# Kernel optimization log

Measured on AMD Instinct MI355X. Metric: run time of the kernel, lower is better.

Reference implementation:

```python
import jax, jax.numpy as jnp
import numpy as np

N_USER = 100000
N_ITEM = 100000
N_EDGE = 1600000
IN_U = 128
IN_I = 128
OUT = 64
NEG_SLOPE = 0.01  # torch F.leaky_relu default


def setup_inputs() -> dict:
    key = jax.random.key(0)
    ks = jax.random.split(key, 12)
    return {
        'feat_user': jax.random.normal(ks[0], (N_USER, IN_U), jnp.float32),
        'feat_item': jax.random.normal(ks[1], (N_ITEM, IN_I), jnp.float32),
        'W_user': jax.random.normal(ks[2], (IN_U, OUT), jnp.float32) * 0.05,
        'b_user': jax.random.normal(ks[3], (OUT,), jnp.float32) * 0.05,
        'W_item': jax.random.normal(ks[4], (IN_I, OUT), jnp.float32) * 0.05,
        'b_item': jax.random.normal(ks[5], (OUT,), jnp.float32) * 0.05,
        'attn_w': jax.random.normal(ks[6], (2 * OUT, 1), jnp.float32) * 0.05,
        'src_u2i': jax.random.randint(ks[7], (N_EDGE,), 0, N_USER),
        'dst_u2i': jax.random.randint(ks[8], (N_EDGE,), 0, N_ITEM),
        'src_i2u': jax.random.randint(ks[9], (N_EDGE,), 0, N_ITEM),
        'dst_i2u': jax.random.randint(ks[10], (N_EDGE,), 0, N_USER),
    }


def _segment_softmax(e, seg, num_segments):
    # e: [E], seg: [E] destination ids -> softmax over edges sharing a dst
    m = jax.ops.segment_max(e, seg, num_segments=num_segments)
    ex = jnp.exp(e - m[seg])
    s = jax.ops.segment_sum(ex, seg, num_segments=num_segments)
    return ex / s[seg]


def _etype_aggregate(Wh_src, Wh_dst, attn_w, src, dst, n_dst):
    # gather per-edge src/dst projected features: [E, OUT]
    zs = Wh_src[src]
    zd = Wh_dst[dst]
    # attn([zs || zd]) == zs @ a_src + zd @ a_dst (split the 2*OUT weight)
    a_src, a_dst = attn_w[:OUT, 0], attn_w[OUT:, 0]
    e = zs @ a_src + zd @ a_dst  # [E]
    e = jnp.where(e > 0, e, NEG_SLOPE * e)  # leaky_relu
    alpha = _segment_softmax(e, dst, n_dst)  # [E]
    # weighted scatter-sum into destination nodes
    return jax.ops.segment_sum(alpha[:, None] * zs, dst, num_segments=n_dst)


def reference(feat_user, feat_item, W_user, b_user, W_item, b_item, attn_w,
              src_u2i, dst_u2i, src_i2u, dst_i2u):
    Wh_user = feat_user @ W_user + b_user  # fc['user'] (etype 'user': user->item)
    Wh_item = feat_item @ W_item + b_item  # fc['item'] (etype 'item': item->user)
    # etype 'user': user -> item; dst attention feature is Wh_item on item nodes
    h_item = _etype_aggregate(Wh_user, Wh_item, attn_w, src_u2i, dst_u2i, N_ITEM)
    # etype 'item': item -> user
    h_user = _etype_aggregate(Wh_item, Wh_user, attn_w, src_i2u, dst_i2u, N_USER)
    # update_nodes sums all 'self_*' per ntype; each ntype has exactly one here
    return jnp.concatenate([h_user, h_item], axis=0)  # [N_USER+N_ITEM, OUT]
```

## Files before the change

### kernel.cpp

```cpp
#include <hip/hip_runtime.h>
#include <hip/hip_bf16.h>

#define NU 100000
#define NI 100000
#define NE 1600000
#define KIN 128
#define KOUT 64

#define NCOPY 8
#define PBK 128
#define NP 782
#define CAP2 384
#define CHUNK 4096
#define SRTSZ (NCOPY * CAP2 + PBK * 7)
#define AGG_THREADS 512
#define NWAVE 8

#define LIN_ROWS 64
#define LIN_GRID 512
#define LIN_ITERS 1563

__device__ __forceinline__ unsigned short f2bf(float f) {
    unsigned u = __float_as_uint(f);
    unsigned r = (u + 0x7fffu + ((u >> 16) & 1u)) >> 16;
    return (unsigned short)r;
}
__device__ __forceinline__ float bf2f(unsigned short h) {
    return __uint_as_float(((unsigned)h) << 16);
}

__global__ __launch_bounds__(256) void linear_attn_kernel(
    const float* __restrict__ A0, const float* __restrict__ W0, const float* __restrict__ bv0,
    const float* __restrict__ A1, const float* __restrict__ W1, const float* __restrict__ bv1,
    const float* __restrict__ attn,
    unsigned short* __restrict__ Wh0, float* __restrict__ su0, float* __restrict__ sd0,
    unsigned short* __restrict__ Wh1, float* __restrict__ su1, float* __restrict__ sd1)
{
    __shared__ float Wl[128 * 64];
    __shared__ float Al[LIN_ROWS * 132];

    int half = gridDim.x >> 1;
    bool second = blockIdx.x >= (unsigned)half;
    const float* A = second ? A1 : A0;
    const float* W = second ? W1 : W0;
    const float* bvec = second ? bv1 : bv0;
    unsigned short* Wh = second ? Wh1 : Wh0;
    float* s_src = second ? su1 : su0;
    float* s_dst = second ? sd1 : sd0;
    int blk = second ? (blockIdx.x - half) : blockIdx.x;

    int t = threadIdx.x;
    int c4 = t & 15;
    int rt = t >> 4;

    for (int i = t; i < 128 * 64 / 4; i += 256) ((float4*)Wl)[i] = ((const float4*)W)[i];

    float4 bias4 = *(const float4*)(bvec + c4 * 4);
    float4 as4   = *(const float4*)(attn + c4 * 4);
    float4 ad4   = *(const float4*)(attn + 64 + c4 * 4);

    for (int c = blk; c < LIN_ITERS; c += half) {
        int rowbase = c * LIN_ROWS;
        __syncthreads();
        for (int g = t; g < LIN_ROWS * 32; g += 256) {
            int rr = g >> 5;
            int q  = g & 31;
            float4 v = {0.f, 0.f, 0.f, 0.f};
            int grow = rowbase + rr;
            if (grow < NU) v = ((const float4*)(A + (size_t)grow * 128))[q];
            *(float4*)&Al[rr * 132 + q * 4] = v;
        }
        __syncthreads();

        float4 acc0 = bias4, acc1 = bias4, acc2 = bias4, acc3 = bias4;
        const float* Ar = &Al[rt * 132];
        const float* Wc = &Wl[c4 * 4];
        #pragma unroll 4
        for (int kq = 0; kq < 128; kq += 4) {
            float4 a0 = *(const float4*)&Ar[ 0 * 132 + kq];
            float4 a1 = *(const float4*)&Ar[16 * 132 + kq];
            float4 a2 = *(const float4*)&Ar[32 * 132 + kq];
            float4 a3 = *(const float4*)&Ar[48 * 132 + kq];
            float4 w0 = *(const float4*)&Wc[(kq + 0) * 64];
            float4 w1 = *(const float4*)&Wc[(kq + 1) * 64];
            float4 w2 = *(const float4*)&Wc[(kq + 2) * 64];
            float4 w3 = *(const float4*)&Wc[(kq + 3) * 64];
            acc0.x += a0.x*w0.x + a0.y*w1.x + a0.z*w2.x + a0.w*w3.x;
            acc0.y += a0.x*w0.y + a0.y*w1.y + a0.z*w2.y + a0.w*w3.y;
            acc0.z += a0.x*w0.z + a0.y*w1.z + a0.z*w2.z + a0.w*w3.z;
            acc0.w += a0.x*w0.w + a0.y*w1.w + a0.z*w2.w + a0.w*w3.w;
            acc1.x += a1.x*w0.x + a1.y*w1.x + a1.z*w2.x + a1.w*w3.x;
            acc1.y += a1.x*w0.y + a1.y*w1.y + a1.z*w2.y + a1.w*w3.y;
            acc1.z += a1.x*w0.z + a1.y*w1.z + a1.z*w2.z + a1.w*w3.z;
            acc1.w += a1.x*w0.w + a1.y*w1.w + a1.z*w2.w + a1.w*w3.w;
            acc2.x += a2.x*w0.x + a2.y*w1.x + a2.z*w2.x + a2.w*w3.x;
            acc2.y += a2.x*w0.y + a2.y*w1.y + a2.z*w2.y + a2.w*w3.y;
            acc2.z += a2.x*w0.z + a2.y*w1.z + a2.z*w2.z + a2.w*w3.z;
            acc2.w += a2.x*w0.w + a2.y*w1.w + a2.z*w2.w + a2.w*w3.w;
            acc3.x += a3.x*w0.x + a3.y*w1.x + a3.z*w2.x + a3.w*w3.x;
            acc3.y += a3.x*w0.y + a3.y*w1.y + a3.z*w2.y + a3.w*w3.y;
            acc3.z += a3.x*w0.z + a3.y*w1.z + a3.z*w2.z + a3.w*w3.z;
            acc3.w += a3.x*w0.w + a3.y*w1.w + a3.z*w2.w + a3.w*w3.w;
        }

        float4 accs[4] = {acc0, acc1, acc2, acc3};
        #pragma unroll
        for (int i = 0; i < 4; i++) {
            int row = rowbase + rt + 16 * i;
            float4 av = accs[i];
            if (row < NU) {
                ushort4 o;
                o.x = f2bf(av.x); o.y = f2bf(av.y); o.z = f2bf(av.z); o.w = f2bf(av.w);
                ((ushort4*)(Wh + (size_t)row * KOUT))[c4] = o;
            }
            float p1 = av.x*as4.x + av.y*as4.y + av.z*as4.z + av.w*as4.w;
            float p2 = av.x*ad4.x + av.y*ad4.y + av.z*ad4.z + av.w*ad4.w;
            #pragma unroll
            for (int off = 8; off; off >>= 1) {
                p1 += __shfl_down(p1, off, 16);
                p2 += __shfl_down(p2, off, 16);
            }
            if (c4 == 0 && row < NU) { s_src[row] = p1; s_dst[row] = p2; }
        }
    }
}

__global__ __launch_bounds__(256) void scatter_kernel(
    const int* __restrict__ src_u2i, const int* __restrict__ dst_u2i,
    const int* __restrict__ src_i2u, const int* __restrict__ dst_i2u,
    int* __restrict__ cur_item, int* __restrict__ cur_user,
    int* __restrict__ ebuf_item, int* __restrict__ ebuf_user,
    int nE, int nbs)
{
    __shared__ int raw[CHUNK];
    __shared__ unsigned short bkt[CHUNK];
    __shared__ int srt_[CHUNK];
    __shared__ unsigned short sbk[CHUNK];
    __shared__ int cnt[NP];
    __shared__ int gb[NP];
    __shared__ int pb[NP];
    __shared__ int lc[NP];

    bool u2i = blockIdx.x < (unsigned)nbs;
    int blk = u2i ? blockIdx.x : (blockIdx.x - nbs);
    int copy = blockIdx.x & (NCOPY - 1);
    const int* src = u2i ? src_u2i : src_i2u;
    const int* dst = u2i ? dst_u2i : dst_i2u;
    int* cur  = (u2i ? cur_item : cur_user) + copy * NP;
    int* ebuf = (u2i ? ebuf_item : ebuf_user) + (size_t)copy * NP * CAP2;

    int t = threadIdx.x;
    for (int i = t; i < NP; i += 256) cnt[i] = 0;
    __syncthreads();

    int e0 = blk * CHUNK;
    int n = nE - e0; if (n > CHUNK) n = CHUNK;

    for (int j = t; j < n; j += 256) {
        int s = src[e0 + j], d = dst[e0 + j];
        int b = d >> 7;
        raw[j] = s | ((d & 127) << 17);
        bkt[j] = (unsigned short)b;
        atomicAdd(&cnt[b], 1);
    }
    __syncthreads();

    for (int b = t; b < NP; b += 256) {
        int c = cnt[b];
        gb[b] = c ? atomicAdd(&cur[b], c) : 0;
    }
    if (t < 64) {
        int lo = t * 13;
        int hi = lo + 13; if (hi > NP) hi = NP; if (lo > NP) lo = NP;
        int s = 0;
        for (int i = lo; i < hi; i++) s += cnt[i];
        int run = s;
        #pragma unroll
        for (int off = 1; off < 64; off <<= 1) {
            int v = __shfl_up(run, off);
            if (t >= off) run += v;
        }
        int excl = run - s;
        for (int i = lo; i < hi; i++) {
            pb[i] = excl; lc[i] = excl;
            excl += cnt[i];
        }
    }
    __syncthreads();

    for (int j = t; j < n; j += 256) {
        int b = bkt[j];
        int p = atomicAdd(&lc[b], 1);
        srt_[p] = raw[j];
        sbk[p] = (unsigned short)b;
    }
    __syncthreads();

    for (int j = t; j < n; j += 256) {
        int b = sbk[j];
        int pos = gb[b] + (j - pb[b]);
        if (pos < CAP2) ebuf[(size_t)b * CAP2 + pos] = srt_[j];
    }
}

__global__ __launch_bounds__(AGG_THREADS) void agg_kernel(
    const int* __restrict__ cur_item, const int* __restrict__ cur_user,
    const int* __restrict__ ebuf_item, const int* __restrict__ ebuf_user,
    const float* __restrict__ su_user, const float* __restrict__ sd_item,
    const float* __restrict__ su_item, const float* __restrict__ sd_user,
    const unsigned short* __restrict__ Wh_user, const unsigned short* __restrict__ Wh_item,
    float* __restrict__ h_item, float* __restrict__ h_user)
{
    __shared__ int   raw[SRTSZ];
    __shared__ int   srt[SRTSZ];
    __shared__ int   offs[NCOPY + 1];
    __shared__ int   cnt[PBK];
    __shared__ int   base[PBK + 1];
    __shared__ int   cursor[PBK];
    __shared__ float sdl[PBK];

    int bid = blockIdx.x;
    bool item_side = bid < NP;
    int b = item_side ? bid : bid - NP;
    const int*   cur  = item_side ? cur_item : cur_user;
    const int*   ebuf = item_side ? ebuf_item : ebuf_user;
    const float* ssrc = item_side ? su_user : su_item;
    const float* sdst = item_side ? sd_item : sd_user;
    const unsigned short* Whs = item_side ? Wh_user : Wh_item;
    float* h = item_side ? h_item : h_user;

    int t = threadIdx.x;
    if (t < PBK) {
        cnt[t] = 0;
        int node = b * PBK + t;
        sdl[t] = (node < NU) ? sdst[node] : 0.f;
    }
    if (t == 0) {
        int a = 0;
        #pragma unroll
        for (int c = 0; c < NCOPY; c++) {
            offs[c] = a;
            int cc = cur[c * NP + b];
            if (cc > CAP2) cc = CAP2;
            a += cc;
        }
        offs[NCOPY] = a;
    }
    for (int j = t; j < SRTSZ; j += AGG_THREADS) srt[j] = 0;
    __syncthreads();

    int total = offs[NCOPY];

    for (int j = t; j < total; j += AGG_THREADS) {
        int c = 0;
        while (j >= offs[c + 1]) c++;
        int e = ebuf[((size_t)c * NP + b) * CAP2 + (j - offs[c])];
        raw[j] = e;
        atomicAdd(&cnt[e >> 17], 1);
    }
    __syncthreads();

    if (t == 0) {
        int a = 0;
        for (int i = 0; i < PBK; i++) {
            base[i] = a; cursor[i] = a;
            a += (cnt[i] + 7) & ~7;
        }
        base[PBK] = a;
    }
    __syncthreads();

    for (int j = t; j < total; j += AGG_THREADS) {
        int e = raw[j];
        int p = atomicAdd(&cursor[e >> 17], 1);
        srt[p] = e;
    }
    __syncthreads();

    int lane = t & 63;
    int wv = t >> 6;

    float* wgt = (float*)raw;
    for (int dl = wv; dl < PBK; dl += NWAVE) {
        int jb = base[dl], cc = cnt[dl], pc = base[dl + 1] - jb;
        float sd = sdl[dl];
        for (int k = lane; k < pc; k += 64) {
            float w = 0.f;
            if (k < cc) {
                int s = srt[jb + k] & 0x1FFFF;
                float ev = ssrc[s] + sd;
                ev = ev > 0.f ? ev : 0.01f * ev;
                w = __expf(ev);
            }
            wgt[jb + k] = w;
        }
    }
    __syncthreads();

    int sub = lane >> 4;
    int ch4 = (lane & 15) << 2;
    const unsigned short* WhCh = Whs + ch4;
    for (int dl = wv; dl < PBK; dl += NWAVE) {
        int node = b * PBK + dl;
        if (node >= NU) break;
        int jb = base[dl];
        int pc = base[dl + 1] - jb;
        int cc = cnt[dl];
        float ax = 0.f, ay = 0.f, az = 0.f, aw = 0.f, ssum = 0.f;
        for (int q = 0; q < pc; q += 8) {
            int j0 = jb + q + sub;
            int j1 = j0 + 4;
            int e0 = srt[j0];
            int e1 = srt[j1];
            float w0 = wgt[j0];
            float w1 = wgt[j1];
            uint2 u0 = *(const uint2*)(WhCh + ((size_t)(e0 & 0x1FFFF) << 6));
            uint2 u1 = *(const uint2*)(WhCh + ((size_t)(e1 & 0x1FFFF) << 6));
            ax += w0 * __uint_as_float(u0.x << 16)        + w1 * __uint_as_float(u1.x << 16);
            ay += w0 * __uint_as_float(u0.x & 0xffff0000u)+ w1 * __uint_as_float(u1.x & 0xffff0000u);
            az += w0 * __uint_as_float(u0.y << 16)        + w1 * __uint_as_float(u1.y << 16);
            aw += w0 * __uint_as_float(u0.y & 0xffff0000u)+ w1 * __uint_as_float(u1.y & 0xffff0000u);
            ssum += w0 + w1;
        }
        #pragma unroll
        for (int off = 16; off <= 32; off <<= 1) {
            ax += __shfl_xor(ax, off);
            ay += __shfl_xor(ay, off);
            az += __shfl_xor(az, off);
            aw += __shfl_xor(aw, off);
            ssum += __shfl_xor(ssum, off);
        }
        if (sub == 0) {
            float inv = (cc > 0) ? 1.f / ssum : 0.f;
            float4 o = {ax * inv, ay * inv, az * inv, aw * inv};
            *(float4*)(h + (size_t)node * KOUT + ch4) = o;
        }
    }
}

extern "C" void kernel_launch(void* const* d_in, const int* in_sizes, int n_in,
                              void* d_out, int out_size, void* d_ws, size_t ws_size,
                              hipStream_t stream)
{
    const float* feat_user = (const float*)d_in[0];
    const float* feat_item = (const float*)d_in[1];
    const float* W_user    = (const float*)d_in[2];
    const float* b_user    = (const float*)d_in[3];
    const float* W_item    = (const float*)d_in[4];
    const float* b_item    = (const float*)d_in[5];
    const float* attn_w    = (const float*)d_in[6];
    const int*   src_u2i   = (const int*)d_in[7];
    const int*   dst_u2i   = (const int*)d_in[8];
    const int*   src_i2u   = (const int*)d_in[9];
    const int*   dst_i2u   = (const int*)d_in[10];

    float* out    = (float*)d_out;
    float* h_user = out;
    float* h_item = out + (size_t)NU * KOUT;

    char* p = (char*)d_ws;
    unsigned short* Wh_user = (unsigned short*)p; p += (size_t)NU * KOUT * 2;
    unsigned short* Wh_item = (unsigned short*)p; p += (size_t)NI * KOUT * 2;
    float* su_user = (float*)p; p += NU * 4;
    float* sd_user = (float*)p; p += NU * 4;
    float* su_item = (float*)p; p += NI * 4;
    float* sd_item = (float*)p; p += NI * 4;
    int* cur_item  = (int*)p; p += (size_t)NCOPY * NP * 4;
    int* cur_user  = (int*)p; p += (size_t)NCOPY * NP * 4;
    int* ebuf_item = (int*)p; p += (size_t)NCOPY * NP * CAP2 * 4;
    int* ebuf_user = (int*)p; p += (size_t)NCOPY * NP * CAP2 * 4;

    hipMemsetAsync(cur_item, 0, (size_t)2 * NCOPY * NP * 4, stream);

    int nbs = (NE + CHUNK - 1) / CHUNK;
    scatter_kernel<<<2 * nbs, 256, 0, stream>>>(src_u2i, dst_u2i, src_i2u, dst_i2u,
                                                cur_item, cur_user, ebuf_item, ebuf_user,
                                                NE, nbs);
    linear_attn_kernel<<<LIN_GRID, 256, 0, stream>>>(feat_user, W_user, b_user,
                                                     feat_item, W_item, b_item, attn_w,
                                                     Wh_user, su_user, sd_user,
                                                     Wh_item, su_item, sd_item);
    agg_kernel<<<2 * NP, AGG_THREADS, 0, stream>>>(cur_item, cur_user, ebuf_item, ebuf_user,
                                                   su_user, sd_item, su_item, sd_user,
                                                   Wh_user, Wh_item, h_item, h_user);
}
```

Measured before the change: 347.7 us.

## Compute node projection GEMM with split-bf16 MFMA instead of FP32 FMA

Replaces the scalar FP32 dot-product loop in the linear/attention-score kernel with MFMA 16x16x32 bf16 instructions. Each FP32 value is split into hi and lo bf16 parts and three MFMAs per tile are used to approximate FP32 accuracy. The weights are pre-split into a packed LDS layout, and the epilogue is rewritten for the MFMA output layout. This targets the compute cost of the projection part of the pipeline, but adds conversion work per A element and narrower scattered 2-byte stores, and the full operation is a mix of several kernels.

```diff
diff --git a/kernel.cpp b/kernel.cpp
--- a/kernel.cpp
+++ b/kernel.cpp
@@ -20,6 +20,9 @@
 #define LIN_GRID 512
 #define LIN_ITERS 1563
 
+typedef short bf16x8 __attribute__((ext_vector_type(8)));
+typedef float f32x4  __attribute__((ext_vector_type(4)));
+
 __device__ __forceinline__ unsigned short f2bf(float f) {
     unsigned u = __float_as_uint(f);
     unsigned r = (u + 0x7fffu + ((u >> 16) & 1u)) >> 16;
@@ -27,6 +30,11 @@
 }
 __device__ __forceinline__ float bf2f(unsigned short h) {
     return __uint_as_float(((unsigned)h) << 16);
+}
+__device__ __forceinline__ void split_bf16(float f, unsigned short& h, unsigned short& l) {
+    h = f2bf(f);
+    float r = f - bf2f(h);
+    l = f2bf(r);
 }
 
 __global__ __launch_bounds__(256) void linear_attn_kernel(
@@ -36,8 +44,9 @@
     unsigned short* __restrict__ Wh0, float* __restrict__ su0, float* __restrict__ sd0,
     unsigned short* __restrict__ Wh1, float* __restrict__ su1, float* __restrict__ sd1)
 {
-    __shared__ float Wl[128 * 64];
     __shared__ float Al[LIN_ROWS * 132];
+    __shared__ __align__(16) unsigned short Wph[4 * 4 * 64 * 8];
+    __shared__ __align__(16) unsigned short Wpl[4 * 4 * 64 * 8];
 
     int half = gridDim.x >> 1;
     bool second = blockIdx.x >= (unsigned)half;
@@ -50,14 +59,36 @@
     int blk = second ? (blockIdx.x - half) : blockIdx.x;
 
     int t = threadIdx.x;
-    int c4 = t & 15;
-    int rt = t >> 4;
-
-    for (int i = t; i < 128 * 64 / 4; i += 256) ((float4*)Wl)[i] = ((const float4*)W)[i];
-
-    float4 bias4 = *(const float4*)(bvec + c4 * 4);
-    float4 as4   = *(const float4*)(attn + c4 * 4);
-    float4 ad4   = *(const float4*)(attn + 64 + c4 * 4);
+    int l   = t & 63;
+    int wv  = t >> 6;
+    int ln  = l & 15;
+    int grp = l >> 4;
+
+    for (int i = 0; i < 4; i++) {
+        int s = t + 256 * i;
+        int sl = s & 63, nt = (s >> 6) & 3, ks = s >> 8;
+        int kb = ks * 32 + (sl >> 4) * 8;
+        int n  = nt * 16 + (sl & 15);
+        unsigned short h8[8], l8[8];
+        #pragma unroll
+        for (int j = 0; j < 8; j++) {
+            float w = W[(size_t)(kb + j) * KOUT + n];
+            split_bf16(w, h8[j], l8[j]);
+        }
+        int base = ((ks * 4 + nt) * 64 + sl) * 8;
+        #pragma unroll
+        for (int j = 0; j < 8; j++) { Wph[base + j] = h8[j]; Wpl[base + j] = l8[j]; }
+    }
+
+    float asl[4], adl[4], bl4[4];
+    #pragma unroll
+    for (int nt = 0; nt < 4; nt++) {
+        asl[nt] = attn[nt * 16 + ln];
+        adl[nt] = attn[64 + nt * 16 + ln];
+        bl4[nt] = bvec[nt * 16 + ln];
+    }
+
+    int arow = wv * 16 + ln;
 
     for (int c = blk; c < LIN_ITERS; c += half) {
         int rowbase = c * LIN_ROWS;
@@ -72,55 +103,58 @@
         }
         __syncthreads();
 
-        float4 acc0 = bias4, acc1 = bias4, acc2 = bias4, acc3 = bias4;
-        const float* Ar = &Al[rt * 132];
-        const float* Wc = &Wl[c4 * 4];
-        #pragma unroll 4
-        for (int kq = 0; kq < 128; kq += 4) {
-            float4 a0 = *(const float4*)&Ar[ 0 * 132 + kq];
-            float4 a1 = *(const float4*)&Ar[16 * 132 + kq];
-            float4 a2 = *(const float4*)&Ar[32 * 132 + kq];
-            float4 a3 = *(const float4*)&Ar[48 * 132 + kq];
-            float4 w0 = *(const float4*)&Wc[(kq + 0) * 64];
-            float4 w1 = *(const float4*)&Wc[(kq + 1) * 64];
-            float4 w2 = *(const float4*)&Wc[(kq + 2) * 64];
-            float4 w3 = *(const float4*)&Wc[(kq + 3) * 64];
-            acc0.x += a0.x*w0.x + a0.y*w1.x + a0.z*w2.x + a0.w*w3.x;
-            acc0.y += a0.x*w0.y + a0.y*w1.y + a0.z*w2.y + a0.w*w3.y;
-            acc0.z += a0.x*w0.z + a0.y*w1.z + a0.z*w2.z + a0.w*w3.z;
-            acc0.w += a0.x*w0.w + a0.y*w1.w + a0.z*w2.w + a0.w*w3.w;
-            acc1.x += a1.x*w0.x + a1.y*w1.x + a1.z*w2.x + a1.w*w3.x;
-            acc1.y += a1.x*w0.y + a1.y*w1.y + a1.z*w2.y + a1.w*w3.y;
-            acc1.z += a1.x*w0.z + a1.y*w1.z + a1.z*w2.z + a1.w*w3.z;
-            acc1.w += a1.x*w0.w + a1.y*w1.w + a1.z*w2.w + a1.w*w3.w;
-            acc2.x += a2.x*w0.x + a2.y*w1.x + a2.z*w2.x + a2.w*w3.x;
-            acc2.y += a2.x*w0.y + a2.y*w1.y + a2.z*w2.y + a2.w*w3.y;
-            acc2.z += a2.x*w0.z + a2.y*w1.z + a2.z*w2.z + a2.w*w3.z;
-            acc2.w += a2.x*w0.w + a2.y*w1.w + a2.z*w2.w + a2.w*w3.w;
-            acc3.x += a3.x*w0.x + a3.y*w1.x + a3.z*w2.x + a3.w*w3.x;
-            acc3.y += a3.x*w0.y + a3.y*w1.y + a3.z*w2.y + a3.w*w3.y;
-            acc3.z += a3.x*w0.z + a3.y*w1.z + a3.z*w2.z + a3.w*w3.z;
-            acc3.w += a3.x*w0.w + a3.y*w1.w + a3.z*w2.w + a3.w*w3.w;
-        }
-
-        float4 accs[4] = {acc0, acc1, acc2, acc3};
-        #pragma unroll
-        for (int i = 0; i < 4; i++) {
-            int row = rowbase + rt + 16 * i;
-            float4 av = accs[i];
-            if (row < NU) {
-                ushort4 o;
-                o.x = f2bf(av.x); o.y = f2bf(av.y); o.z = f2bf(av.z); o.w = f2bf(av.w);
-                ((ushort4*)(Wh + (size_t)row * KOUT))[c4] = o;
+        f32x4 acc0 = {bl4[0], bl4[0], bl4[0], bl4[0]};
+        f32x4 acc1 = {bl4[1], bl4[1], bl4[1], bl4[1]};
+        f32x4 acc2 = {bl4[2], bl4[2], bl4[2], bl4[2]};
+        f32x4 acc3 = {bl4[3], bl4[3], bl4[3], bl4[3]};
+
+        #pragma unroll
+        for (int ks = 0; ks < 4; ks++) {
+            int k0 = ks * 32 + grp * 8;
+            const float* ap = &Al[arow * 132 + k0];
+            float4 va = *(const float4*)ap;
+            float4 vb = *(const float4*)(ap + 4);
+            float av[8] = {va.x, va.y, va.z, va.w, vb.x, vb.y, vb.z, vb.w};
+            bf16x8 ahi, alo;
+            #pragma unroll
+            for (int j = 0; j < 8; j++) {
+                unsigned short h, lo2;
+                split_bf16(av[j], h, lo2);
+                ahi[j] = (short)h; alo[j] = (short)lo2;
             }
-            float p1 = av.x*as4.x + av.y*as4.y + av.z*as4.z + av.w*as4.w;
-            float p2 = av.x*ad4.x + av.y*ad4.y + av.z*ad4.z + av.w*ad4.w;
             #pragma unroll
-            for (int off = 8; off; off >>= 1) {
-                p1 += __shfl_down(p1, off, 16);
-                p2 += __shfl_down(p2, off, 16);
+            for (int nt = 0; nt < 4; nt++) {
+                bf16x8 bhi = *(const bf16x8*)&Wph[((ks * 4 + nt) * 64 + l) * 8];
+                bf16x8 blo = *(const bf16x8*)&Wpl[((ks * 4 + nt) * 64 + l) * 8];
+                f32x4 a = (nt == 0) ? acc0 : (nt == 1) ? acc1 : (nt == 2) ? acc2 : acc3;
+                a = __builtin_amdgcn_mfma_f32_16x16x32_bf16(ahi, bhi, a, 0, 0, 0);
+                a = __builtin_amdgcn_mfma_f32_16x16x32_bf16(ahi, blo, a, 0, 0, 0);
+                a = __builtin_amdgcn_mfma_f32_16x16x32_bf16(alo, bhi, a, 0, 0, 0);
+                if (nt == 0) acc0 = a; else if (nt == 1) acc1 = a; else if (nt == 2) acc2 = a; else acc3 = a;
             }
-            if (c4 == 0 && row < NU) { s_src[row] = p1; s_dst[row] = p2; }
+        }
+
+        int growbase = rowbase + wv * 16;
+        f32x4 accs[4] = {acc0, acc1, acc2, acc3};
+        #pragma unroll
+        for (int nt = 0; nt < 4; nt++) {
+            #pragma unroll
+            for (int r = 0; r < 4; r++) {
+                int row = growbase + grp * 4 + r;
+                if (row < NU) Wh[(size_t)row * KOUT + nt * 16 + ln] = f2bf(accs[nt][r]);
+            }
+        }
+        #pragma unroll
+        for (int r = 0; r < 4; r++) {
+            float p1 = accs[0][r] * asl[0] + accs[1][r] * asl[1] + accs[2][r] * asl[2] + accs[3][r] * asl[3];
+            float p2 = accs[0][r] * adl[0] + accs[1][r] * adl[1] + accs[2][r] * adl[2] + accs[3][r] * adl[3];
+            #pragma unroll
+            for (int off = 1; off < 16; off <<= 1) {
+                p1 += __shfl_xor(p1, off);
+                p2 += __shfl_xor(p2, off);
+            }
+            int row = growbase + grp * 4 + r;
+            if (ln == 0 && row < NU) { s_src[row] = p1; s_dst[row] = p2; }
         }
     }
 }
```

Result: faster. 317.9 us (-8.6%).
